# Optimization experiments

Measured on AMD Instinct MI355X. Metric: run time of the kernel, lower is better.

## Reference

```python
import jax, jax.numpy as jnp
import numpy as np
from jax.scipy.special import gammaln

N, F, P = 65536, 256, 4194304
PARAM_RES = 1e-12          # param_resolution_scale
W_MODEL = 1.0              # weight_model_bits
EPS = float(np.finfo(np.float32).eps * 5)
HALF_LOG2_2PIE = 0.5 * float(np.log2(2.0 * np.pi * np.e))
LAMBDA_BITS = 2.0 * float(np.log2(100.0))
LN2 = float(np.log(2.0))


def nanmedian(x):
    """torch.nanmedian semantics for 1-D x: lower median of finite values; nan if none."""
    finite = jnp.isfinite(x)
    m = finite.sum()
    xs = jnp.sort(jnp.where(finite, x, jnp.inf))
    idx = jnp.maximum((m - 1) // 2, 0)
    med = xs[idx]
    return jnp.where(m == 0, jnp.nan, med)


def feature_resolution(x):
    """Median positive gap between sorted finite values, clamped to [1e-12, 0.1]."""
    finite = jnp.isfinite(x)
    xs = jnp.sort(jnp.where(finite, x, jnp.inf))
    diffs = xs[1:] - xs[:-1]
    pos = jnp.where(diffs > 1e-12, diffs, jnp.nan)
    res = nanmedian(pos)
    valid = jnp.where(jnp.isfinite(res), res, 1e-6)
    final = jnp.clip(valid, 1e-12, 0.1)
    return jnp.where(finite.sum() < 2, jnp.asarray(1e-6, x.dtype), final)


def feature_bits(y, log_jac, resolution):
    finite = jnp.isfinite(y)
    n_f = finite.sum().astype(y.dtype)
    n = jnp.asarray(y.size, y.dtype)
    n_ex = n - n_f
    yc = jnp.where(finite, y, 0.0)
    mean = yc.sum() / jnp.maximum(n_f, 1.0)
    sq = jnp.where(finite, (y - mean) ** 2, 0.0)
    var = jnp.maximum(sq.sum() / jnp.maximum(n_f, 1.0), 1e-12)
    diff_bits = jnp.where(n_f > 1, n_f * (HALF_LOG2_2PIE + 0.5 * jnp.log2(var)), 0.0)
    lj_sum = jnp.where(finite, log_jac, 0.0).sum() / LN2
    lj_bits = jnp.where(n_f > 0, lj_sum, 0.0)
    ex_bits = jnp.where(n_ex > 0, n_ex * jnp.log2(1.0 / resolution), 0.0)
    has_partial = (n_ex > 0) & (n_ex < n)
    log_binom = jnp.where(
        has_partial,
        gammaln(n + 1.0) - gammaln(n_ex + 1.0) - gammaln(n - n_ex + 1.0),
        0.0,
    )
    part_bits = jnp.where(has_partial, log_binom / LN2, 0.0)
    return diff_bits + lj_bits + ex_bits + part_bits + LAMBDA_BITS


def two_param_yeo_johnson(x, lam1, lam2):
    """x:[N], lam1/lam2 scalars -> (y:[N], log_jac:[N])."""
    pos = x >= 0
    xp = jnp.where(pos, x, 0.0)           # safe input for positive branch
    xn = jnp.where(pos, 0.0, x)           # safe input for negative branch
    l1z = jnp.abs(lam1) < EPS
    l1s = jnp.where(l1z, 1.0, lam1)       # avoid div-by-zero in unselected branch
    lp = jnp.log1p(xp)
    y_pos = jnp.where(l1z, lp, ((1.0 + xp) ** l1s - 1.0) / l1s)
    lj_pos = jnp.where(l1z, -lp, (lam1 - 1.0) * lp)
    l2t = jnp.abs(lam2 - 2.0) < EPS
    two_m = jnp.where(l2t, 1.0, 2.0 - lam2)
    base = jnp.maximum(1.0 - xn, 1e-18)
    ln = jnp.log1p(-xn)
    y_neg = jnp.where(l2t, -ln, -((base ** two_m - 1.0) / two_m))
    lj_neg = jnp.where(l2t, -ln, (1.0 - lam2) * jnp.log(base))
    y = jnp.where(pos, y_pos, y_neg)
    lj = jnp.where(pos, lj_pos, lj_neg)
    return y, lj


def _feature_total_bits(x_col, lam1, lam2, rp):
    """One SA step for one feature: evaluate current + 5 proposals, pick best, emit bits.
    (feature_complexity in the original is computed but unused -> omitted.)"""
    res = feature_resolution(x_col)  # depends only on x_col; shared by all proposals
    std_dev = 0.1  # 0.1 * temperature(=1.0)
    all_l1 = jnp.concatenate([lam1[None], lam1 + std_dev * rp[0::2]])  # [6]
    all_l2 = jnp.concatenate([lam2[None], lam2 + std_dev * rp[1::2]])  # [6]

    def score(l1, l2):
        y, lj = two_param_yeo_johnson(x_col, l1, l2)
        return feature_bits(y, lj, res)

    scores = jax.vmap(score)(all_l1, all_l2)  # [6]
    mn = scores.min()
    w = (scores == mn).astype(x_col.dtype)
    tw = jnp.maximum(w.sum(), 1e-8)
    best_l1 = (all_l1 * w).sum() / tw
    best_l2 = (all_l2 * w).sum() / tw
    y, lj = two_param_yeo_johnson(x_col, best_l1, best_l2)
    return feature_bits(y, lj, res)


def setup_inputs() -> dict:
    key = jax.random.key(0)
    k1, k2, k3 = jax.random.split(key, 3)
    return {
        "x": jax.random.normal(k1, (N, F), dtype=jnp.float32),
        "lam1": jnp.ones((F,), dtype=jnp.float32),
        "lam2": jnp.ones((F,), dtype=jnp.float32),
        "random_proposals": jax.random.normal(k2, (F, 10), dtype=jnp.float32),
        "params": jax.random.normal(k3, (P,), dtype=jnp.float32),
    }


def reference(x, lam1, lam2, random_proposals, params):
    # data bits: per-feature SA pipeline, vmapped over features
    per_feat = jax.vmap(_feature_total_bits)(x.T, lam1, lam2, random_proposals)  # [F]
    data_bits = per_feat.sum()
    # model bits: parameter tensor as a feature with fixed resolution, zero log-Jacobian
    model_bits = feature_bits(params, jnp.zeros_like(params), jnp.asarray(PARAM_RES, params.dtype))
    return data_bits + W_MODEL * model_bits
```

## Files before the change

kernel.cpp:

```cpp
#include <hip/hip_runtime.h>
#include <math.h>

#define NFEAT 256
#define NROWS 65536
#define PCOUNT 4194304
#define PBLK 64
#define CH2 512
#define RGRP 16
#define NSLOT 28
#define F_EPS 5.9604645e-07f
#define F_LN2 0.69314718056f
#define DELTA_MAX 0.45f

#define FAST_LOG2(v) __builtin_log2f(v)
#define FAST_EXP2(v) __builtin_exp2f(v)

constexpr double D_HALF_LOG2_2PIE = 0.5 * 2.8378770664093453 / 0.6931471805599453;
constexpr double D_LAMBDA_BITS = 13.287712379549449;

__device__ inline double wave_reduce_add(double v) {
  for (int o = 32; o > 0; o >>= 1) v += __shfl_down(v, o, 64);
  return v;
}

__device__ inline double horner_exp(const double* m, double d) {
  double p = m[5] * (1.0 / 120.0);
  p = p * d + m[4] * (1.0 / 24.0);
  p = p * d + m[3] * (1.0 / 6.0);
  p = p * d + m[2] * 0.5;
  p = p * d + m[1];
  p = p * d + m[0];
  return p;
}

__global__ __launch_bounds__(512, 8) void k_pass1(
    const float* __restrict__ x, const float* __restrict__ lam1,
    const float* __restrict__ lam2, const float* __restrict__ rp,
    const float* __restrict__ params, float* __restrict__ P1,
    double* __restrict__ pSums, int CHv, int rpt)
{
  const int tid = threadIdx.x;
  const int nyj = CHv >> 1;

  if ((int)blockIdx.x >= nyj) {
    __shared__ double lred[2][8];
    const int b = blockIdx.x - nyj;
    const float4* p4 = (const float4*)params;
    double s = 0.0, q = 0.0;
    for (int i = b * 512 + tid; i < PCOUNT / 4; i += PBLK * 512) {
      float4 v = p4[i];
      s += (double)v.x + (double)v.y + (double)v.z + (double)v.w;
      q += (double)v.x * v.x + (double)v.y * v.y
         + (double)v.z * v.z + (double)v.w * v.w;
    }
    s = wave_reduce_add(s); q = wave_reduce_add(q);
    const int w = tid >> 6;
    if ((tid & 63) == 0) { lred[0][w] = s; lred[1][w] = q; }
    __syncthreads();
    if (tid == 0) {
      double S = 0.0, Q = 0.0;
#pragma unroll
      for (int i = 0; i < 8; ++i) { S += lred[0][i]; Q += lred[1][i]; }
      atomicAdd(&pSums[0], S);
      atomicAdd(&pSums[1], Q);
    }
    return;
  }

  const int f = tid & 255;
  const int sub = tid >> 8;
  const int c = blockIdx.x * 2 + sub;
  __shared__ int bad;
  if (tid == 0) bad = 0;
  __syncthreads();

  const float L1 = lam1[f], L2 = lam2[f];
  const float An = 2.0f - L2;
  {
    bool b = (fabsf(L1) < F_EPS) || (fabsf(An) < F_EPS);
#pragma unroll
    for (int j = 1; j < 6; ++j) {
      float dp = 0.1f * rp[f * 10 + 2 * (j - 1)];
      float dn = -0.1f * rp[f * 10 + 2 * (j - 1) + 1];
      b = b || (fabsf(L1 + dp) < F_EPS) || (fabsf(An + dn) < F_EPS)
            || (fabsf(dp) > DELTA_MAX) || (fabsf(dn) > DELTA_MAX);
    }
    if (b) bad = 1;
  }
  __syncthreads();

  const float* xp = x + (size_t)c * rpt * NFEAT + f;
  float out[NSLOT];

  if (bad == 0) {
    float Mp[6], Mp2[6], Mn[6], Mn2[6];
#pragma unroll
    for (int k = 0; k < 6; ++k) { Mp[k] = 0.f; Mp2[k] = 0.f; Mn[k] = 0.f; Mn2[k] = 0.f; }
    float u2p = 0.f, u2a = 0.f, npos = 0.f;

#pragma unroll 4
    for (int i = 0; i < rpt; ++i) {
      const float v = xp[(size_t)i * NFEAT];
      const bool pos = v >= 0.0f;
      const float u = FAST_LOG2(1.0f + fabsf(v));
      u2a += u;
      u2p += pos ? u : 0.0f;
      npos += pos ? 1.0f : 0.0f;
      const float q = u * F_LN2;
      const float B = FAST_EXP2((pos ? L1 : An) * u);
      const float B2 = B * B;
      const float Bp = pos ? B : 0.0f;
      const float Bn = B - Bp;
      const float Cp = pos ? B2 : 0.0f;
      const float Cn = B2 - Cp;
      Mp[0] += Bp; Mp2[0] += Cp; Mn[0] += Bn; Mn2[0] += Cn;
      float qk = q;
      Mp[1] = fmaf(Bp, qk, Mp[1]); Mp2[1] = fmaf(Cp, qk, Mp2[1]);
      Mn[1] = fmaf(Bn, qk, Mn[1]); Mn2[1] = fmaf(Cn, qk, Mn2[1]);
#pragma unroll
      for (int k = 2; k < 6; ++k) {
        qk *= q;
        Mp[k] = fmaf(Bp, qk, Mp[k]); Mp2[k] = fmaf(Cp, qk, Mp2[k]);
        Mn[k] = fmaf(Bn, qk, Mn[k]); Mn2[k] = fmaf(Cn, qk, Mn2[k]);
      }
    }
#pragma unroll
    for (int k = 0; k < 6; ++k) {
      out[k]      = Mp[k];
      out[6 + k]  = Mp2[k];
      out[12 + k] = Mn[k];
      out[18 + k] = Mn2[k];
    }
    out[24] = u2p; out[25] = u2a; out[26] = npos; out[27] = 0.0f;
  } else {
    float ga_p[6], ga_n[6], gs_p[6], gs_n[6], gt_p[6], gt_n[6];
#pragma unroll
    for (int j = 0; j < 6; ++j) {
      float dp = (j == 0) ? 0.0f : 0.1f * rp[f * 10 + 2 * (j - 1)];
      float dn = (j == 0) ? 0.0f : -0.1f * rp[f * 10 + 2 * (j - 1) + 1];
      float a1 = L1 + dp;
      float a2 = An + dn;
      bool z1 = fabsf(a1) < F_EPS;
      bool z2 = fabsf(a2) < F_EPS;
      ga_p[j] = z1 ? 0.0f : a1;
      gs_p[j] = z1 ? 0.0f : 1.0f / a1;
      gt_p[j] = z1 ? F_LN2 : 0.0f;
      ga_n[j] = z2 ? 0.0f : a2;
      gs_n[j] = z2 ? 0.0f : -1.0f / a2;
      gt_n[j] = z2 ? -F_LN2 : 0.0f;
    }
    float as[6], aq[6];
#pragma unroll
    for (int j = 0; j < 6; ++j) { as[j] = 0.f; aq[j] = 0.f; }
    float u2p = 0.f, u2a = 0.f;
    for (int i = 0; i < rpt; ++i) {
      float v = xp[(size_t)i * NFEAT];
      bool pos = v >= 0.0f;
      float u2 = FAST_LOG2(1.0f + fabsf(v));
      u2a += u2;
      u2p += pos ? u2 : 0.0f;
#pragma unroll
      for (int j = 0; j < 6; ++j) {
        float a  = pos ? ga_p[j] : ga_n[j];
        float s  = pos ? gs_p[j] : gs_n[j];
        float tt = pos ? gt_p[j] : gt_n[j];
        float e = FAST_EXP2(a * u2);
        float y = fmaf(tt, u2, fmaf(s, e, -s));
        as[j] += y;
        aq[j] = fmaf(y, y, aq[j]);
      }
    }
#pragma unroll
    for (int k = 0; k < NSLOT; ++k) out[k] = 0.0f;
#pragma unroll
    for (int j = 0; j < 6; ++j) { out[j] = as[j]; out[6 + j] = aq[j]; }
    out[24] = u2p; out[25] = u2a; out[26] = 0.0f; out[27] = 1.0f;
  }

#pragma unroll
  for (int k = 0; k < NSLOT; ++k)
    P1[((size_t)c * NSLOT + k) * NFEAT + f] = out[k];
}

__global__ __launch_bounds__(256) void k_reduce_S(
    const float* __restrict__ P1, double* __restrict__ S2, int CHv)
{
  const int k = blockIdx.x / RGRP;
  const int cg = blockIdx.x % RGRP;
  const int f = threadIdx.x;
  const int per = CHv / RGRP;
  const int c0 = cg * per;
  double a0 = 0.0, a1 = 0.0, a2 = 0.0, a3 = 0.0;
  for (int c = c0; c < c0 + per; c += 4) {
    a0 += (double)P1[((size_t)(c + 0) * NSLOT + k) * NFEAT + f];
    a1 += (double)P1[((size_t)(c + 1) * NSLOT + k) * NFEAT + f];
    a2 += (double)P1[((size_t)(c + 2) * NSLOT + k) * NFEAT + f];
    a3 += (double)P1[((size_t)(c + 3) * NSLOT + k) * NFEAT + f];
  }
  S2[((size_t)k * RGRP + cg) * NFEAT + f] = (a0 + a1) + (a2 + a3);
}

__global__ __launch_bounds__(256) void k_pick(
    const double* __restrict__ S2, const float* __restrict__ lam1,
    const float* __restrict__ lam2, const float* __restrict__ rp,
    float* __restrict__ bestL, int* __restrict__ tied,
    double* __restrict__ bitsF, int* __restrict__ anyTied)
{
  const int f = threadIdx.x;
  if (f == 0) *anyTied = 0;
  double s[NSLOT];
#pragma unroll
  for (int k = 0; k < NSLOT; ++k) {
    double a = 0.0;
#pragma unroll
    for (int cg = 0; cg < RGRP; ++cg)
      a += S2[((size_t)k * RGRP + cg) * NFEAT + f];
    s[k] = a;
  }
  const double n = (double)NROWS;
  const bool direct = s[27] > 0.5;
  const double npos = s[26];
  const double nneg = n - npos;
  const double sup = s[24];
  const double sun = s[25] - s[24];
  const float L1 = lam1[f], L2 = lam2[f];
  const double dAn = 2.0 - (double)L2;
  double scores[6], al1[6], al2[6];
#pragma unroll
  for (int j = 0; j < 6; ++j) {
    float l1 = (j == 0) ? L1 : L1 + 0.1f * rp[f * 10 + 2 * (j - 1)];
    float l2 = (j == 0) ? L2 : L2 + 0.1f * rp[f * 10 + 2 * (j - 1) + 1];
    al1[j] = (double)l1; al2[j] = (double)l2;
    bool z1 = fabsf(l1) < F_EPS;
    bool z2 = fabsf(l2 - 2.0f) < F_EPS;
    double ccp = z1 ? -1.0 : (double)l1 - 1.0;
    double ccn = z2 ? -1.0 : 1.0 - (double)l2;
    double ljb = ccp * sup + ccn * sun;

    double sum_y, sum_y2;
    if (direct) {
      sum_y  = s[j];
      sum_y2 = s[6 + j];
    } else {
      const double dp  = (double)l1 - (double)L1;
      const double dnn = (2.0 - (double)l2) - dAn;
      const double sp = 1.0 / ((double)L1 + dp);
      const double sn = -1.0 / (dAn + dnn);
      const double Ep  = horner_exp(&s[0],  dp);
      const double Ep2 = horner_exp(&s[6],  2.0 * dp);
      const double En  = horner_exp(&s[12], dnn);
      const double En2 = horner_exp(&s[18], 2.0 * dnn);
      sum_y  = sp * (Ep - npos) + sn * (En - nneg);
      sum_y2 = sp * sp * (Ep2 - 2.0 * Ep + npos)
             + sn * sn * (En2 - 2.0 * En + nneg);
    }
    double mean = sum_y / n;
    double var = sum_y2 / n - mean * mean;
    var = var > 1e-12 ? var : 1e-12;
    scores[j] = n * (D_HALF_LOG2_2PIE + 0.5 * log2(var)) + ljb + D_LAMBDA_BITS;
  }
  double mn = scores[0];
#pragma unroll
  for (int j = 1; j < 6; ++j) mn = scores[j] < mn ? scores[j] : mn;
  double wsum = 0.0, b1 = 0.0, b2 = 0.0;
#pragma unroll
  for (int j = 0; j < 6; ++j) {
    double w = (scores[j] == mn) ? 1.0 : 0.0;
    wsum += w; b1 += w * al1[j]; b2 += w * al2[j];
  }
  bestL[2 * f]     = (float)(b1 / wsum);
  bestL[2 * f + 1] = (float)(b2 / wsum);
  const int isTied = (wsum > 1.5) ? 1 : 0;
  tied[f] = isTied;
  if (isTied) atomicOr(anyTied, 1);
  bitsF[f] = mn;
}

__global__ __launch_bounds__(256) void k_pass2(
    const float* __restrict__ x, const float* __restrict__ bestL,
    const int* __restrict__ anyTied, float* __restrict__ P2)
{
  if (*anyTied == 0) return;
  const int t = threadIdx.x;
  const int c = blockIdx.x;
  const int rpt = NROWS / CH2;
  const float l1 = bestL[2 * t], l2 = bestL[2 * t + 1];
  const bool z1 = fabsf(l1) < F_EPS;
  const bool z2 = fabsf(l2 - 2.0f) < F_EPS;
  const float tm = 2.0f - l2;
  const float a_p = z1 ? 0.f : l1,  s_pv = z1 ? 0.f : 1.f / l1,  t_pv = z1 ? F_LN2 : 0.f;
  const float a_n = z2 ? 0.f : tm,  s_nv = z2 ? 0.f : -1.f / tm, t_nv = z2 ? -F_LN2 : 0.f;

  float sy = 0.f, sq = 0.f;
  const float* xp = x + (size_t)c * rpt * NFEAT + t;
  for (int i = 0; i < rpt; ++i) {
    float v = xp[(size_t)i * NFEAT];
    bool pos = v >= 0.0f;
    float u2 = FAST_LOG2(1.0f + fabsf(v));
    float a  = pos ? a_p : a_n;
    float s  = pos ? s_pv : s_nv;
    float tt = pos ? t_pv : t_nv;
    float e = FAST_EXP2(a * u2);
    float y = fmaf(tt, u2, fmaf(s, e, -s));
    sy += y;
    sq = fmaf(y, y, sq);
  }
  P2[((size_t)c * 2 + 0) * NFEAT + t] = sy;
  P2[((size_t)c * 2 + 1) * NFEAT + t] = sq;
}

__global__ __launch_bounds__(64) void k_featbits(
    const float* __restrict__ P1, const float* __restrict__ P2,
    const float* __restrict__ bestL, const int* __restrict__ tied,
    double* __restrict__ bitsF, int CHv)
{
  const int f = blockIdx.x;
  if (!tied[f]) return;
  const int lane = threadIdx.x;
  double s0 = 0.0, s1 = 0.0, sup = 0.0, sua = 0.0;
  for (int c = lane; c < CH2; c += 64) {
    s0 += (double)P2[((size_t)c * 2 + 0) * NFEAT + f];
    s1 += (double)P2[((size_t)c * 2 + 1) * NFEAT + f];
  }
  for (int c = lane; c < CHv; c += 64) {
    sup += (double)P1[((size_t)c * NSLOT + 24) * NFEAT + f];
    sua += (double)P1[((size_t)c * NSLOT + 25) * NFEAT + f];
  }
  s0 = wave_reduce_add(s0); s1 = wave_reduce_add(s1);
  sup = wave_reduce_add(sup); sua = wave_reduce_add(sua);
  if (lane == 0) {
    const float l1 = bestL[2 * f], l2 = bestL[2 * f + 1];
    bool z1 = fabsf(l1) < F_EPS;
    bool z2 = fabsf(l2 - 2.0f) < F_EPS;
    double ccp = z1 ? -1.0 : (double)l1 - 1.0;
    double ccn = z2 ? -1.0 : 1.0 - (double)l2;
    double ljb = ccp * sup + ccn * (sua - sup);
    const double n = (double)NROWS;
    double mean = s0 / n;
    double var = s1 / n - mean * mean;
    var = var > 1e-12 ? var : 1e-12;
    bitsF[f] = n * (D_HALF_LOG2_2PIE + 0.5 * log2(var)) + ljb + D_LAMBDA_BITS;
  }
}

__global__ __launch_bounds__(256) void k_final(
    const double* __restrict__ bitsF, const double* __restrict__ pSums,
    float* __restrict__ out)
{
  __shared__ double l[4];
  double s = bitsF[threadIdx.x];
  s = wave_reduce_add(s);
  int w = threadIdx.x >> 6;
  if ((threadIdx.x & 63) == 0) l[w] = s;
  __syncthreads();
  if (threadIdx.x == 0) {
    double data = l[0] + l[1] + l[2] + l[3];
    const double n = (double)PCOUNT;
    double mean = pSums[0] / n;
    double var = pSums[1] / n - mean * mean;
    var = var > 1e-12 ? var : 1e-12;
    double model = n * (D_HALF_LOG2_2PIE + 0.5 * log2(var)) + D_LAMBDA_BITS;
    out[0] = (float)(data + model);
  }
}

extern "C" void kernel_launch(void* const* d_in, const int* in_sizes, int n_in,
                              void* d_out, int out_size, void* d_ws, size_t ws_size,
                              hipStream_t stream)
{
  const float* x      = (const float*)d_in[0];
  const float* lam1   = (const float*)d_in[1];
  const float* lam2   = (const float*)d_in[2];
  const float* rp     = (const float*)d_in[3];
  const float* params = (const float*)d_in[4];

  char* ws = (char*)d_ws;
  double* pSums  = (double*)ws;
  float*  bestL  = (float*)(ws + 16);
  double* bitsF  = (double*)(ws + 2064);
  int*    tied   = (int*)(ws + 4112);
  int*    anyT   = (int*)(ws + 5136);
  double* S2     = (double*)(ws + 5152);
  float*  P1     = (float*)(ws + 922656);

  int CHv = 1024;
  while (CHv > 128) {
    size_t need = 922656 + (size_t)CHv * NSLOT * NFEAT * 4
                         + (size_t)CH2 * 2 * NFEAT * 4;
    if (need <= ws_size) break;
    CHv >>= 1;
  }
  float* P2 = (float*)(ws + 922656 + (size_t)CHv * NSLOT * NFEAT * 4);
  int rpt = NROWS / CHv;

  (void)hipMemsetAsync(pSums, 0, 16, stream);
  k_pass1<<<CHv / 2 + PBLK, 512, 0, stream>>>(x, lam1, lam2, rp, params, P1,
                                              pSums, CHv, rpt);
  k_reduce_S<<<NSLOT * RGRP, 256, 0, stream>>>(P1, S2, CHv);
  k_pick<<<1, 256, 0, stream>>>(S2, lam1, lam2, rp, bestL, tied, bitsF, anyT);
  k_pass2<<<CH2, 256, 0, stream>>>(x, bestL, anyT, P2);
  k_featbits<<<NFEAT, 64, 0, stream>>>(P1, P2, bestL, tied, bitsF, CHv);
  k_final<<<1, 256, 0, stream>>>(bitsF, pSums, (float*)d_out);
}
```

Baseline: 70.85 us.

## Combine block-local partials in LDS and replace atomics with per-block partial sums

In pass1, the two 256-thread halves of each block now add their 28-slot partials through shared memory, so each block writes one set instead of two. This halves the P1 intermediate buffer and the traffic in the following reduce kernel, whose group count drops from 16 to 4. The params sum/sum-of-squares now go to per-block slots reduced in k_final, which removes the double atomics and the memset launch. The cost is an extra 28 KB of LDS per block and a barrier at the end of pass1, which may lower occupancy, and fewer reduce blocks means less parallelism in that kernel.

```diff
diff --git a/kernel.cpp b/kernel.cpp
--- a/kernel.cpp
+++ b/kernel.cpp
@@ -6,7 +6,7 @@
 #define PCOUNT 4194304
 #define PBLK 64
 #define CH2 512
-#define RGRP 16
+#define RGRP 4
 #define NSLOT 28
 #define F_EPS 5.9604645e-07f
 #define F_LN2 0.69314718056f
@@ -37,10 +37,9 @@
     const float* __restrict__ x, const float* __restrict__ lam1,
     const float* __restrict__ lam2, const float* __restrict__ rp,
     const float* __restrict__ params, float* __restrict__ P1,
-    double* __restrict__ pSums, int CHv, int rpt)
+    double* __restrict__ pPart, int nyj, int rpt)
 {
   const int tid = threadIdx.x;
-  const int nyj = CHv >> 1;
 
   if ((int)blockIdx.x >= nyj) {
     __shared__ double lred[2][8];
@@ -61,8 +60,8 @@
       double S = 0.0, Q = 0.0;
 #pragma unroll
       for (int i = 0; i < 8; ++i) { S += lred[0][i]; Q += lred[1][i]; }
-      atomicAdd(&pSums[0], S);
-      atomicAdd(&pSums[1], Q);
+      pPart[2 * b]     = S;
+      pPart[2 * b + 1] = Q;
     }
     return;
   }
@@ -70,6 +69,7 @@
   const int f = tid & 255;
   const int sub = tid >> 8;
   const int c = blockIdx.x * 2 + sub;
+  __shared__ float red[NSLOT][NFEAT];
   __shared__ int bad;
   if (tid == 0) bad = 0;
   __syncthreads();
@@ -177,18 +177,25 @@
     out[24] = u2p; out[25] = u2a; out[26] = 0.0f; out[27] = 1.0f;
   }
 
-#pragma unroll
-  for (int k = 0; k < NSLOT; ++k)
-    P1[((size_t)c * NSLOT + k) * NFEAT + f] = out[k];
+  if (sub == 1) {
+#pragma unroll
+    for (int k = 0; k < NSLOT; ++k) red[k][f] = out[k];
+  }
+  __syncthreads();
+  if (sub == 0) {
+#pragma unroll
+    for (int k = 0; k < NSLOT; ++k)
+      P1[((size_t)blockIdx.x * NSLOT + k) * NFEAT + f] = out[k] + red[k][f];
+  }
 }
 
 __global__ __launch_bounds__(256) void k_reduce_S(
-    const float* __restrict__ P1, double* __restrict__ S2, int CHv)
+    const float* __restrict__ P1, double* __restrict__ S2, int nsets)
 {
   const int k = blockIdx.x / RGRP;
   const int cg = blockIdx.x % RGRP;
   const int f = threadIdx.x;
-  const int per = CHv / RGRP;
+  const int per = nsets / RGRP;
   const int c0 = cg * per;
   double a0 = 0.0, a1 = 0.0, a2 = 0.0, a3 = 0.0;
   for (int c = c0; c < c0 + per; c += 4) {
@@ -312,7 +319,7 @@
 __global__ __launch_bounds__(64) void k_featbits(
     const float* __restrict__ P1, const float* __restrict__ P2,
     const float* __restrict__ bestL, const int* __restrict__ tied,
-    double* __restrict__ bitsF, int CHv)
+    double* __restrict__ bitsF, int nsets)
 {
   const int f = blockIdx.x;
   if (!tied[f]) return;
@@ -322,7 +329,7 @@
     s0 += (double)P2[((size_t)c * 2 + 0) * NFEAT + f];
     s1 += (double)P2[((size_t)c * 2 + 1) * NFEAT + f];
   }
-  for (int c = lane; c < CHv; c += 64) {
+  for (int c = lane; c < nsets; c += 64) {
     sup += (double)P1[((size_t)c * NSLOT + 24) * NFEAT + f];
     sua += (double)P1[((size_t)c * NSLOT + 25) * NFEAT + f];
   }
@@ -344,20 +351,25 @@
 }
 
 __global__ __launch_bounds__(256) void k_final(
-    const double* __restrict__ bitsF, const double* __restrict__ pSums,
+    const double* __restrict__ bitsF, const double* __restrict__ pPart,
     float* __restrict__ out)
 {
-  __shared__ double l[4];
-  double s = bitsF[threadIdx.x];
-  s = wave_reduce_add(s);
-  int w = threadIdx.x >> 6;
-  if ((threadIdx.x & 63) == 0) l[w] = s;
+  __shared__ double l[4], lp[4], lq[4];
+  const int t = threadIdx.x;
+  double s  = bitsF[t];
+  double sp = (t < PBLK) ? pPart[2 * t]     : 0.0;
+  double sq = (t < PBLK) ? pPart[2 * t + 1] : 0.0;
+  s = wave_reduce_add(s); sp = wave_reduce_add(sp); sq = wave_reduce_add(sq);
+  const int w = t >> 6;
+  if ((t & 63) == 0) { l[w] = s; lp[w] = sp; lq[w] = sq; }
   __syncthreads();
-  if (threadIdx.x == 0) {
+  if (t == 0) {
     double data = l[0] + l[1] + l[2] + l[3];
+    double S = lp[0] + lp[1] + lp[2] + lp[3];
+    double Q = lq[0] + lq[1] + lq[2] + lq[3];
     const double n = (double)PCOUNT;
-    double mean = pSums[0] / n;
-    double var = pSums[1] / n - mean * mean;
+    double mean = S / n;
+    double var = Q / n - mean * mean;
     var = var > 1e-12 ? var : 1e-12;
     double model = n * (D_HALF_LOG2_2PIE + 0.5 * log2(var)) + D_LAMBDA_BITS;
     out[0] = (float)(data + model);
@@ -375,30 +387,29 @@
   const float* params = (const float*)d_in[4];
 
   char* ws = (char*)d_ws;
-  double* pSums  = (double*)ws;
-  float*  bestL  = (float*)(ws + 16);
-  double* bitsF  = (double*)(ws + 2064);
-  int*    tied   = (int*)(ws + 4112);
-  int*    anyT   = (int*)(ws + 5136);
-  double* S2     = (double*)(ws + 5152);
-  float*  P1     = (float*)(ws + 922656);
-
-  int CHv = 1024;
-  while (CHv > 128) {
-    size_t need = 922656 + (size_t)CHv * NSLOT * NFEAT * 4
+  double* pPart = (double*)ws;
+  float*  bestL = (float*)(ws + 1024);
+  double* bitsF = (double*)(ws + 3072);
+  int*    tied  = (int*)(ws + 5120);
+  int*    anyT  = (int*)(ws + 6144);
+  double* S2    = (double*)(ws + 6176);
+  float*  P1    = (float*)(ws + 235552);
+
+  int nsets = 512;
+  while (nsets > 64) {
+    size_t need = 235552 + (size_t)nsets * NSLOT * NFEAT * 4
                          + (size_t)CH2 * 2 * NFEAT * 4;
     if (need <= ws_size) break;
-    CHv >>= 1;
-  }
-  float* P2 = (float*)(ws + 922656 + (size_t)CHv * NSLOT * NFEAT * 4);
-  int rpt = NROWS / CHv;
-
-  (void)hipMemsetAsync(pSums, 0, 16, stream);
-  k_pass1<<<CHv / 2 + PBLK, 512, 0, stream>>>(x, lam1, lam2, rp, params, P1,
-                                              pSums, CHv, rpt);
-  k_reduce_S<<<NSLOT * RGRP, 256, 0, stream>>>(P1, S2, CHv);
+    nsets >>= 1;
+  }
+  float* P2 = (float*)(ws + 235552 + (size_t)nsets * NSLOT * NFEAT * 4);
+  int rpt = NROWS / (2 * nsets);
+
+  k_pass1<<<nsets + PBLK, 512, 0, stream>>>(x, lam1, lam2, rp, params, P1,
+                                            pPart, nsets, rpt);
+  k_reduce_S<<<NSLOT * RGRP, 256, 0, stream>>>(P1, S2, nsets);
   k_pick<<<1, 256, 0, stream>>>(S2, lam1, lam2, rp, bestL, tied, bitsF, anyT);
   k_pass2<<<CH2, 256, 0, stream>>>(x, bestL, anyT, P2);
-  k_featbits<<<NFEAT, 64, 0, stream>>>(P1, P2, bestL, tied, bitsF, CHv);
-  k_final<<<1, 256, 0, stream>>>(bitsF, pSums, (float*)d_out);
-}
+  k_featbits<<<NFEAT, 64, 0, stream>>>(P1, P2, bestL, tied, bitsF, nsets);
+  k_final<<<1, 256, 0, stream>>>(bitsF, pPart, (float*)d_out);
+}
```

After: 59.30 us (median of 2 runs). -16.3%, faster.
